# Kernel tuning notes

Measured on AMD Instinct MI355X. Metric: run time of the kernel, lower is better.

Reference implementation:

```python
import jax, jax.numpy as jnp
import numpy as np

B, S, D, H = 2, 2048, 2048, 16
DK = D // H  # 128


def setup_inputs() -> dict:
    key = jax.random.key(0)
    ks = jax.random.split(key, 14)
    scale = 1.0 / np.sqrt(D)
    inp = {
        "query": jax.random.normal(ks[0], (B, S, D), jnp.float32),
        "key": jax.random.normal(ks[1], (B, S, D), jnp.float32),
        "value": jax.random.normal(ks[2], (B, S, D), jnp.float32),
        # Linear params, torch convention: y = x @ W.T + b, W:[out,in]
        "Wq": jax.random.normal(ks[3], (D, D), jnp.float32) * scale,
        "bq": jnp.zeros((D,), jnp.float32),
        "Wk": jax.random.normal(ks[4], (D, D), jnp.float32) * scale,
        "bk": jnp.zeros((D,), jnp.float32),
        "Wv": jax.random.normal(ks[5], (D, D), jnp.float32) * scale,
        "bv": jnp.zeros((D,), jnp.float32),
        "Wo": jax.random.normal(ks[6], (D, D), jnp.float32) * scale,
        "bo": jnp.zeros((D,), jnp.float32),
    }
    return inp


def reference(query, key, value, Wq, bq, Wk, bk, Wv, bv, Wo, bo):
    b, s, d = query.shape
    # QKV projections -> [B, H, S, DK]
    q = (query @ Wq.T + bq).reshape(b, s, H, DK).transpose(0, 2, 1, 3)
    k = (key @ Wk.T + bk).reshape(b, s, H, DK).transpose(0, 2, 1, 3)
    v = (value @ Wv.T + bv).reshape(b, s, H, DK).transpose(0, 2, 1, 3)
    # scaled dot-product scores [B, H, S, S]
    scores = jnp.einsum('bhqd,bhkd->bhqk', q, k) * (1.0 / np.sqrt(DK))
    causal = jnp.tril(jnp.ones((s, s), dtype=bool))  # [S, S], mask==0 above diag
    scores = jnp.where(causal[None, None], scores, jnp.float32(-1e9))
    attn = jax.nn.softmax(scores, axis=-1)  # attn_dropout = identity (eval)
    x = jnp.einsum('bhqk,bhkd->bhqd', attn, v)
    x = x.transpose(0, 2, 1, 3).reshape(b, s, d)
    out = x @ Wo.T + bo  # resid_dropout = identity (eval)
    return (out, attn)
```

## Files before the change

kernel.cpp:

```cpp
#include <hip/hip_runtime.h>


#define BATCH 2
#define S_LEN 2048
#define D_DIM 2048
#define H_NUM 16
#define DKD   128
#define NEL   ((size_t)BATCH * S_LEN * D_DIM)
#define NWL   ((size_t)D_DIM * D_DIM)

typedef __attribute__((ext_vector_type(8))) short  short8;
typedef __attribute__((ext_vector_type(4))) short  short4v;
typedef __attribute__((ext_vector_type(4))) float  floatx4;

__device__ __forceinline__ unsigned short f2bf(float f) {
    unsigned int u = __float_as_uint(f);
    u += 0x7fffu + ((u >> 16) & 1u);
    return (unsigned short)(u >> 16);
}

__device__ __forceinline__ void gload16(const void* g, void* l) {
    __builtin_amdgcn_global_load_lds(
        (const __attribute__((address_space(1))) void*)g,
        (__attribute__((address_space(3))) void*)l, 16, 0, 0);
}

__device__ __forceinline__ void stage_lds_bf16(const unsigned short* __restrict__ src,
                                               int ld, int row0, int k0,
                                               unsigned short* __restrict__ dst,
                                               int tid) {
    #pragma unroll
    for (int j = 0; j < 2; ++j) {
        const int c = tid + j * 256;
        const int r = c >> 2, kc = (c & 3) * 8;
        gload16(src + (size_t)(row0 + r) * ld + k0 + kc, dst + c * 8);
    }
}

__launch_bounds__(256)
__global__ void proj_qkv(const unsigned short* __restrict__ xf,
                         const unsigned short* __restrict__ wb,
                         const float* __restrict__ bq, const float* __restrict__ bk,
                         const float* __restrict__ bv,
                         unsigned short* __restrict__ ob) {
    const int z = blockIdx.z;
    const unsigned short* Ap = xf + (size_t)z * NEL;
    const unsigned short* Bp = wb + (size_t)z * NWL;
    const float* bias = (z == 0) ? bq : (z == 1) ? bk : bv;
    const int m0 = blockIdx.y * 128, n0 = blockIdx.x * 128;

    __shared__ __align__(16) unsigned short As[128][32];
    __shared__ __align__(16) unsigned short Bs[128][32];
    const int tid = threadIdx.x, lane = tid & 63, wave = tid >> 6;
    const int quad = lane >> 4, l16 = lane & 15;
    const int mw = (wave >> 1) * 64, nw = (wave & 1) * 64;

    floatx4 acc[4][4];
    #pragma unroll
    for (int i = 0; i < 4; ++i)
        #pragma unroll
        for (int j = 0; j < 4; ++j) acc[i][j] = (floatx4){0.f, 0.f, 0.f, 0.f};

    for (int k0 = 0; k0 < D_DIM; k0 += 32) {
        if (k0 > 0) __syncthreads();
        stage_lds_bf16(Bp, D_DIM, n0, k0, &Bs[0][0], tid);
        stage_lds_bf16(Ap, D_DIM, m0, k0, &As[0][0], tid);
        __syncthreads();
        short8 af[4], bf[4];
        #pragma unroll
        for (int i = 0; i < 4; ++i) af[i] = *(const short8*)&As[mw + i*16 + l16][quad*8];
        #pragma unroll
        for (int j = 0; j < 4; ++j) bf[j] = *(const short8*)&Bs[nw + j*16 + l16][quad*8];
        #pragma unroll
        for (int i = 0; i < 4; ++i)
            #pragma unroll
            for (int j = 0; j < 4; ++j)
                acc[i][j] = __builtin_amdgcn_mfma_f32_16x16x32_bf16(
                    af[i], bf[j], acc[i][j], 0, 0, 0);
    }

    #pragma unroll
    for (int i = 0; i < 4; ++i)
        #pragma unroll
        for (int j = 0; j < 4; ++j)
            #pragma unroll
            for (int r = 0; r < 4; ++r) {
                const int row = m0 + mw + i*16 + quad*4 + r;
                const int col = n0 + nw + j*16 + l16;
                const float v = acc[i][j][r] + bias[col];
                const int b = row >> 11, s = row & (S_LEN - 1);
                const int h = col >> 7,  dk = col & (DKD - 1);
                if (z < 2) {
                    unsigned short* o = ob + (size_t)z * NEL;
                    o[((size_t)(b * H_NUM + h) * S_LEN + s) * DKD + dk] = f2bf(v);
                } else {
                    unsigned short* o = ob + 2 * NEL;
                    o[((size_t)(b * H_NUM + h) * DKD + dk) * S_LEN + s] = f2bf(v);
                }
            }
}

__launch_bounds__(256)
__global__ void gemm_out(const unsigned short* __restrict__ Ap,
                         const unsigned short* __restrict__ Bp,
                         const float* __restrict__ bias, float* __restrict__ Cg) {
    const int m0 = blockIdx.y * 128, n0 = blockIdx.x * 128;
    __shared__ __align__(16) unsigned short As[128][32];
    __shared__ __align__(16) unsigned short Bs[128][32];
    const int tid = threadIdx.x, lane = tid & 63, wave = tid >> 6;
    const int quad = lane >> 4, l16 = lane & 15;
    const int mw = (wave >> 1) * 64, nw = (wave & 1) * 64;

    floatx4 acc[4][4];
    #pragma unroll
    for (int i = 0; i < 4; ++i)
        #pragma unroll
        for (int j = 0; j < 4; ++j) acc[i][j] = (floatx4){0.f, 0.f, 0.f, 0.f};

    for (int k0 = 0; k0 < D_DIM; k0 += 32) {
        if (k0 > 0) __syncthreads();
        stage_lds_bf16(Bp, D_DIM, n0, k0, &Bs[0][0], tid);
        stage_lds_bf16(Ap, D_DIM, m0, k0, &As[0][0], tid);
        __syncthreads();
        short8 af[4], bf[4];
        #pragma unroll
        for (int i = 0; i < 4; ++i) af[i] = *(const short8*)&As[mw + i*16 + l16][quad*8];
        #pragma unroll
        for (int j = 0; j < 4; ++j) bf[j] = *(const short8*)&Bs[nw + j*16 + l16][quad*8];
        #pragma unroll
        for (int i = 0; i < 4; ++i)
            #pragma unroll
            for (int j = 0; j < 4; ++j)
                acc[i][j] = __builtin_amdgcn_mfma_f32_16x16x32_bf16(
                    af[i], bf[j], acc[i][j], 0, 0, 0);
    }
    #pragma unroll
    for (int i = 0; i < 4; ++i)
        #pragma unroll
        for (int j = 0; j < 4; ++j)
            #pragma unroll
            for (int r = 0; r < 4; ++r) {
                const int row = m0 + mw + i*16 + quad*4 + r;
                const int col = n0 + nw + j*16 + l16;
                Cg[(size_t)row * D_DIM + col] = acc[i][j][r] + bias[col];
            }
}

__launch_bounds__(256)
__global__ void scores_exp(const unsigned short* __restrict__ qb,
                           const unsigned short* __restrict__ kb,
                           float* __restrict__ attn, float* __restrict__ sums,
                           float scale) {
    const int idx = blockIdx.x;
    int mt = (int)((sqrtf(8.f * (float)idx + 1.f) - 1.f) * 0.5f);
    while ((mt + 1) * (mt + 2) / 2 <= idx) ++mt;
    while (mt * (mt + 1) / 2 > idx) --mt;
    const int nt = idx - mt * (mt + 1) / 2;
    const int m0 = mt * 128, n0 = nt * 128;
    const size_t z = blockIdx.z;
    const unsigned short* Ap = qb + z * (size_t)S_LEN * DKD;
    const unsigned short* Bp = kb + z * (size_t)S_LEN * DKD;

    __shared__ __align__(16) unsigned short As[4][128][32];
    __shared__ __align__(16) unsigned short Bs[4][128][32];
    const int tid = threadIdx.x, lane = tid & 63, wave = tid >> 6;
    const int quad = lane >> 4, l16 = lane & 15;
    const int mw = (wave >> 1) * 64, nw = (wave & 1) * 64;

    #pragma unroll
    for (int kk = 0; kk < 4; ++kk) {
        stage_lds_bf16(Ap, DKD, m0, kk * 32, &As[kk][0][0], tid);
        stage_lds_bf16(Bp, DKD, n0, kk * 32, &Bs[kk][0][0], tid);
    }
    __syncthreads();

    floatx4 acc[4][4];
    #pragma unroll
    for (int i = 0; i < 4; ++i)
        #pragma unroll
        for (int j = 0; j < 4; ++j) acc[i][j] = (floatx4){0.f, 0.f, 0.f, 0.f};

    #pragma unroll
    for (int kk = 0; kk < 4; ++kk) {
        short8 af[4], bf[4];
        #pragma unroll
        for (int i = 0; i < 4; ++i) af[i] = *(const short8*)&As[kk][mw + i*16 + l16][quad*8];
        #pragma unroll
        for (int j = 0; j < 4; ++j) bf[j] = *(const short8*)&Bs[kk][nw + j*16 + l16][quad*8];
        #pragma unroll
        for (int i = 0; i < 4; ++i)
            #pragma unroll
            for (int j = 0; j < 4; ++j)
                acc[i][j] = __builtin_amdgcn_mfma_f32_16x16x32_bf16(
                    af[i], bf[j], acc[i][j], 0, 0, 0);
    }

    float* o  = attn + z * (size_t)S_LEN * S_LEN;
    float* sm = sums + z * S_LEN;
    #pragma unroll
    for (int i = 0; i < 4; ++i)
        #pragma unroll
        for (int r = 0; r < 4; ++r) {
            const int row = m0 + mw + i*16 + quad*4 + r;
            float rsum = 0.f;
            #pragma unroll
            for (int j = 0; j < 4; ++j) {
                const int col = n0 + nw + j*16 + l16;
                const float e = (col <= row) ? __expf(acc[i][j][r] * scale) : 0.f;
                o[(size_t)row * S_LEN + col] = e;
                rsum += e;
            }
            rsum += __shfl_xor(rsum, 1, 64);
            rsum += __shfl_xor(rsum, 2, 64);
            rsum += __shfl_xor(rsum, 4, 64);
            rsum += __shfl_xor(rsum, 8, 64);
            if (l16 == 0) atomicAdd(&sm[row], rsum);
        }
}

__launch_bounds__(256)
__global__ void pv_norm(float* __restrict__ attn,
                        const unsigned short* __restrict__ vT,
                        const float* __restrict__ sums,
                        unsigned short* __restrict__ xb) {
    const int mt = (int)gridDim.y - 1 - (int)blockIdx.y;
    const int m0 = mt * 128;
    const size_t z = blockIdx.z;
    float* Sp = attn + z * (size_t)S_LEN * S_LEN;
    const unsigned short* Bp = vT + z * (size_t)DKD * S_LEN;
    const int kEnd = m0 + 128;

    __shared__ __align__(16) unsigned short As[128][32];
    __shared__ __align__(16) unsigned short Bs[128][32];
    __shared__ float inv[128];
    const int tid = threadIdx.x, lane = tid & 63, wave = tid >> 6;
    const int quad = lane >> 4, l16 = lane & 15;
    const int mw = (wave >> 1) * 64, nw = (wave & 1) * 64;

    if (tid < 128) inv[tid] = 1.f / sums[z * S_LEN + m0 + tid];
    __syncthreads();

    floatx4 acc[4][4];
    #pragma unroll
    for (int i = 0; i < 4; ++i)
        #pragma unroll
        for (int j = 0; j < 4; ++j) acc[i][j] = (floatx4){0.f, 0.f, 0.f, 0.f};

    for (int k0 = 0; k0 < kEnd; k0 += 32) {
        if (k0 > 0) __syncthreads();
        stage_lds_bf16(Bp, S_LEN, 0, k0, &Bs[0][0], tid);
        #pragma unroll
        for (int i2 = 0; i2 < 4; ++i2) {
            const int c = tid + i2 * 256;
            const int r = c >> 3, kc = (c & 7) * 4;
            float* p = Sp + (size_t)(m0 + r) * S_LEN + k0 + kc;
            floatx4 v = *(const floatx4*)p;
            const float iv = inv[r];
            floatx4 w;
            w[0] = v[0] * iv; w[1] = v[1] * iv; w[2] = v[2] * iv; w[3] = v[3] * iv;
            *(floatx4*)p = w;
            short4v pk;
            pk[0] = (short)f2bf(w[0]); pk[1] = (short)f2bf(w[1]);
            pk[2] = (short)f2bf(w[2]); pk[3] = (short)f2bf(w[3]);
            *(short4v*)(&As[r][kc]) = pk;
        }
        __syncthreads();
        short8 af[4], bf[4];
        #pragma unroll
        for (int i = 0; i < 4; ++i) af[i] = *(const short8*)&As[mw + i*16 + l16][quad*8];
        #pragma unroll
        for (int j = 0; j < 4; ++j) bf[j] = *(const short8*)&Bs[nw + j*16 + l16][quad*8];
        #pragma unroll
        for (int i = 0; i < 4; ++i)
            #pragma unroll
            for (int j = 0; j < 4; ++j)
                acc[i][j] = __builtin_amdgcn_mfma_f32_16x16x32_bf16(
                    af[i], bf[j], acc[i][j], 0, 0, 0);
    }

    const int b = (int)(z >> 4), h = (int)(z & 15);
    #pragma unroll
    for (int i = 0; i < 4; ++i)
        #pragma unroll
        for (int j = 0; j < 4; ++j)
            #pragma unroll
            for (int r = 0; r < 4; ++r) {
                const int row = m0 + mw + i*16 + quad*4 + r;
                const int col = nw + j*16 + l16;
                xb[((size_t)(b * S_LEN + row)) * D_DIM + h * DKD + col] =
                    f2bf(acc[i][j][r]);
            }

    const int width = S_LEN - kEnd;
    if (width > 0) {
        const floatx4 z4 = {0.f, 0.f, 0.f, 0.f};
        for (int r = 0; r < 128; ++r) {
            float* rp = Sp + (size_t)(m0 + r) * S_LEN + kEnd;
            for (int c = tid * 4; c < width; c += 1024)
                *(floatx4*)(rp + c) = z4;
        }
    }
}

__launch_bounds__(256)
__global__ void cvt3(const float* __restrict__ a, const float* __restrict__ b,
                     const float* __restrict__ c, unsigned short* __restrict__ dst,
                     size_t stride) {
    const float* src = (blockIdx.y == 0) ? a : (blockIdx.y == 1) ? b : c;
    const size_t i = ((size_t)blockIdx.x * 256 + threadIdx.x) * 8;
    const floatx4 x = *(const floatx4*)(src + i);
    const floatx4 y = *(const floatx4*)(src + i + 4);
    short8 o;
    o[0] = (short)f2bf(x[0]); o[1] = (short)f2bf(x[1]);
    o[2] = (short)f2bf(x[2]); o[3] = (short)f2bf(x[3]);
    o[4] = (short)f2bf(y[0]); o[5] = (short)f2bf(y[1]);
    o[6] = (short)f2bf(y[2]); o[7] = (short)f2bf(y[3]);
    *(short8*)(dst + blockIdx.y * stride + i) = o;
}

__launch_bounds__(256)
__global__ void cvt4(const float* __restrict__ a, const float* __restrict__ b,
                     const float* __restrict__ c, const float* __restrict__ d,
                     unsigned short* __restrict__ dst, size_t stride) {
    const float* src = (blockIdx.y == 0) ? a : (blockIdx.y == 1) ? b
                     : (blockIdx.y == 2) ? c : d;
    const size_t i = ((size_t)blockIdx.x * 256 + threadIdx.x) * 8;
    const floatx4 x = *(const floatx4*)(src + i);
    const floatx4 y = *(const floatx4*)(src + i + 4);
    short8 o;
    o[0] = (short)f2bf(x[0]); o[1] = (short)f2bf(x[1]);
    o[2] = (short)f2bf(x[2]); o[3] = (short)f2bf(x[3]);
    o[4] = (short)f2bf(y[0]); o[5] = (short)f2bf(y[1]);
    o[6] = (short)f2bf(y[2]); o[7] = (short)f2bf(y[3]);
    *(short8*)(dst + blockIdx.y * stride + i) = o;
}

__launch_bounds__(256)
__global__ void zero_sums(float* __restrict__ sums) {
    const size_t i = ((size_t)blockIdx.x * 256 + threadIdx.x) * 4;
    *(floatx4*)(sums + i) = (floatx4){0.f, 0.f, 0.f, 0.f};
}

extern "C" void kernel_launch(void* const* d_in, const int* in_sizes, int n_in,
                              void* d_out, int out_size, void* d_ws, size_t ws_size,
                              hipStream_t stream) {
    const float* query = (const float*)d_in[0];
    const float* key_  = (const float*)d_in[1];
    const float* value = (const float*)d_in[2];
    const float* Wq = (const float*)d_in[3];
    const float* bq = (const float*)d_in[4];
    const float* Wk = (const float*)d_in[5];
    const float* bk = (const float*)d_in[6];
    const float* Wv = (const float*)d_in[7];
    const float* bv = (const float*)d_in[8];
    const float* Wo = (const float*)d_in[9];
    const float* bo = (const float*)d_in[10];

    float* out  = (float*)d_out;
    float* attn = out + NEL;

    unsigned short* qb = (unsigned short*)d_ws;
    unsigned short* kb = qb + NEL;
    unsigned short* vT = kb + NEL;
    unsigned short* xb = vT + NEL;
    unsigned short* qf = xb + NEL;
    unsigned short* wq = qf + 3 * NEL;
    unsigned short* wo = wq + 3 * NWL;
    float* sums = (float*)(wo + NWL);

    const dim3 blk(256);
    const float iscale = 0.088388347648318447f;

    cvt3<<<dim3(NEL / 2048, 3), blk, 0, stream>>>(query, key_, value, qf, NEL);
    cvt4<<<dim3(NWL / 2048, 4), blk, 0, stream>>>(Wq, Wk, Wv, Wo, wq, NWL);
    zero_sums<<<dim3((BATCH * H_NUM * S_LEN) / 1024), blk, 0, stream>>>(sums);

    proj_qkv<<<dim3(D_DIM / 128, (BATCH * S_LEN) / 128, 3), blk, 0, stream>>>(
        qf, wq, bq, bk, bv, qb);

    scores_exp<<<dim3(136, 1, BATCH * H_NUM), blk, 0, stream>>>(
        qb, kb, attn, sums, iscale);

    pv_norm<<<dim3(1, S_LEN / 128, BATCH * H_NUM), blk, 0, stream>>>(
        attn, vT, sums, xb);

    gemm_out<<<dim3(D_DIM / 128, (BATCH * S_LEN) / 128), blk, 0, stream>>>(
        xb, wq + 3 * NWL, bo, out);
}
```

Measured before the change: 1.237 ms.

## Fuse scores, softmax and PV into one attention kernel per query block

Replaces the separate scores_exp and pv_norm kernels with a single kernel that works on 32-row query blocks. For each 128-key tile it computes QK^T, exponentiates, writes the unnormalized probabilities, and feeds them as bf16 directly into the PV MFMA. Row sums stay in LDS instead of global atomics, so the zero_sums launch goes away and pv_norm no longer has to re-read attn to build the PV operand. Normalization of the attn output is done in a second pass that re-reads and rewrites the causal part, and zero-filling is folded into the same pass. The costs are smaller tiles with lower MFMA reuse, a row-serial normalization loop, and softmax without max subtraction, as before.

```diff
diff --git a/kernel.cpp b/kernel.cpp
--- a/kernel.cpp
+++ b/kernel.cpp
@@ -6,6 +6,7 @@
 #define D_DIM 2048
 #define H_NUM 16
 #define DKD   128
+#define QBLK  32
 #define NEL   ((size_t)BATCH * S_LEN * D_DIM)
 #define NWL   ((size_t)D_DIM * D_DIM)
 
@@ -147,158 +148,146 @@
 }
 
 __launch_bounds__(256)
-__global__ void scores_exp(const unsigned short* __restrict__ qb,
+__global__ void attn_fused(const unsigned short* __restrict__ qb,
                            const unsigned short* __restrict__ kb,
-                           float* __restrict__ attn, float* __restrict__ sums,
-                           float scale) {
-    const int idx = blockIdx.x;
-    int mt = (int)((sqrtf(8.f * (float)idx + 1.f) - 1.f) * 0.5f);
-    while ((mt + 1) * (mt + 2) / 2 <= idx) ++mt;
-    while (mt * (mt + 1) / 2 > idx) --mt;
-    const int nt = idx - mt * (mt + 1) / 2;
-    const int m0 = mt * 128, n0 = nt * 128;
-    const size_t z = blockIdx.z;
-    const unsigned short* Ap = qb + z * (size_t)S_LEN * DKD;
-    const unsigned short* Bp = kb + z * (size_t)S_LEN * DKD;
-
-    __shared__ __align__(16) unsigned short As[4][128][32];
-    __shared__ __align__(16) unsigned short Bs[4][128][32];
-    const int tid = threadIdx.x, lane = tid & 63, wave = tid >> 6;
+                           const unsigned short* __restrict__ vTg,
+                           float* __restrict__ attn,
+                           unsigned short* __restrict__ xb,
+                           float iscale) {
+    const int bid = blockIdx.x;
+    const int z  = ((bid & 7) << 2) | ((bid >> 3) & 3);
+    const int mt = 63 - (bid >> 5);
+    const int m0 = mt * QBLK;
+    const int nkt = (m0 + QBLK + 127) >> 7;
+    const unsigned short* qz = qb  + (size_t)z * S_LEN * DKD;
+    const unsigned short* kz = kb  + (size_t)z * S_LEN * DKD;
+    const unsigned short* vz = vTg + (size_t)z * DKD * S_LEN;
+    float* az = attn + (size_t)z * S_LEN * S_LEN;
+
+    __shared__ __align__(16) unsigned short Ks[4][128][32];
+    __shared__ __align__(16) unsigned short Vs[4][128][32];
+    __shared__ __align__(16) unsigned short Ps[4][QBLK][32];
+    __shared__ float rsum[QBLK];
+
+    const int tid = threadIdx.x, lane = tid & 63, w = tid >> 6;
     const int quad = lane >> 4, l16 = lane & 15;
-    const int mw = (wave >> 1) * 64, nw = (wave & 1) * 64;
-
-    #pragma unroll
-    for (int kk = 0; kk < 4; ++kk) {
-        stage_lds_bf16(Ap, DKD, m0, kk * 32, &As[kk][0][0], tid);
-        stage_lds_bf16(Bp, DKD, n0, kk * 32, &Bs[kk][0][0], tid);
-    }
-    __syncthreads();
-
-    floatx4 acc[4][4];
-    #pragma unroll
-    for (int i = 0; i < 4; ++i)
-        #pragma unroll
-        for (int j = 0; j < 4; ++j) acc[i][j] = (floatx4){0.f, 0.f, 0.f, 0.f};
-
-    #pragma unroll
-    for (int kk = 0; kk < 4; ++kk) {
-        short8 af[4], bf[4];
-        #pragma unroll
-        for (int i = 0; i < 4; ++i) af[i] = *(const short8*)&As[kk][mw + i*16 + l16][quad*8];
-        #pragma unroll
-        for (int j = 0; j < 4; ++j) bf[j] = *(const short8*)&Bs[kk][nw + j*16 + l16][quad*8];
-        #pragma unroll
-        for (int i = 0; i < 4; ++i)
-            #pragma unroll
-            for (int j = 0; j < 4; ++j)
-                acc[i][j] = __builtin_amdgcn_mfma_f32_16x16x32_bf16(
-                    af[i], bf[j], acc[i][j], 0, 0, 0);
-    }
-
-    float* o  = attn + z * (size_t)S_LEN * S_LEN;
-    float* sm = sums + z * S_LEN;
-    #pragma unroll
-    for (int i = 0; i < 4; ++i)
-        #pragma unroll
-        for (int r = 0; r < 4; ++r) {
-            const int row = m0 + mw + i*16 + quad*4 + r;
-            float rsum = 0.f;
-            #pragma unroll
-            for (int j = 0; j < 4; ++j) {
-                const int col = n0 + nw + j*16 + l16;
-                const float e = (col <= row) ? __expf(acc[i][j][r] * scale) : 0.f;
-                o[(size_t)row * S_LEN + col] = e;
-                rsum += e;
-            }
-            rsum += __shfl_xor(rsum, 1, 64);
-            rsum += __shfl_xor(rsum, 2, 64);
-            rsum += __shfl_xor(rsum, 4, 64);
-            rsum += __shfl_xor(rsum, 8, 64);
-            if (l16 == 0) atomicAdd(&sm[row], rsum);
-        }
-}
-
-__launch_bounds__(256)
-__global__ void pv_norm(float* __restrict__ attn,
-                        const unsigned short* __restrict__ vT,
-                        const float* __restrict__ sums,
-                        unsigned short* __restrict__ xb) {
-    const int mt = (int)gridDim.y - 1 - (int)blockIdx.y;
-    const int m0 = mt * 128;
-    const size_t z = blockIdx.z;
-    float* Sp = attn + z * (size_t)S_LEN * S_LEN;
-    const unsigned short* Bp = vT + z * (size_t)DKD * S_LEN;
-    const int kEnd = m0 + 128;
-
-    __shared__ __align__(16) unsigned short As[128][32];
-    __shared__ __align__(16) unsigned short Bs[128][32];
-    __shared__ float inv[128];
-    const int tid = threadIdx.x, lane = tid & 63, wave = tid >> 6;
-    const int quad = lane >> 4, l16 = lane & 15;
-    const int mw = (wave >> 1) * 64, nw = (wave & 1) * 64;
-
-    if (tid < 128) inv[tid] = 1.f / sums[z * S_LEN + m0 + tid];
-    __syncthreads();
-
-    floatx4 acc[4][4];
-    #pragma unroll
-    for (int i = 0; i < 4; ++i)
-        #pragma unroll
-        for (int j = 0; j < 4; ++j) acc[i][j] = (floatx4){0.f, 0.f, 0.f, 0.f};
-
-    for (int k0 = 0; k0 < kEnd; k0 += 32) {
-        if (k0 > 0) __syncthreads();
-        stage_lds_bf16(Bp, S_LEN, 0, k0, &Bs[0][0], tid);
-        #pragma unroll
-        for (int i2 = 0; i2 < 4; ++i2) {
-            const int c = tid + i2 * 256;
-            const int r = c >> 3, kc = (c & 7) * 4;
-            float* p = Sp + (size_t)(m0 + r) * S_LEN + k0 + kc;
-            floatx4 v = *(const floatx4*)p;
-            const float iv = inv[r];
-            floatx4 w;
-            w[0] = v[0] * iv; w[1] = v[1] * iv; w[2] = v[2] * iv; w[3] = v[3] * iv;
-            *(floatx4*)p = w;
-            short4v pk;
-            pk[0] = (short)f2bf(w[0]); pk[1] = (short)f2bf(w[1]);
-            pk[2] = (short)f2bf(w[2]); pk[3] = (short)f2bf(w[3]);
-            *(short4v*)(&As[r][kc]) = pk;
+
+    if (tid < QBLK) rsum[tid] = 0.f;
+
+    short8 afq[2][4];
+    #pragma unroll
+    for (int i = 0; i < 2; ++i)
+        #pragma unroll
+        for (int kk = 0; kk < 4; ++kk)
+            afq[i][kk] = *(const short8*)(qz + (size_t)(m0 + i*16 + l16) * DKD
+                                             + kk*32 + quad*8);
+
+    floatx4 acc_pv[2][2];
+    #pragma unroll
+    for (int i = 0; i < 2; ++i)
+        #pragma unroll
+        for (int jj = 0; jj < 2; ++jj) acc_pv[i][jj] = (floatx4){0.f,0.f,0.f,0.f};
+    float rp[2][4];
+    #pragma unroll
+    for (int i = 0; i < 2; ++i)
+        #pragma unroll
+        for (int r = 0; r < 4; ++r) rp[i][r] = 0.f;
+
+    for (int kt = 0; kt < nkt; ++kt) {
+        const int k0 = kt * 128;
+        if (kt > 0) __syncthreads();
+        #pragma unroll
+        for (int kk = 0; kk < 4; ++kk) {
+            stage_lds_bf16(kz, DKD,   k0, kk*32,      &Ks[kk][0][0], tid);
+            stage_lds_bf16(vz, S_LEN, 0,  k0 + kk*32, &Vs[kk][0][0], tid);
         }
         __syncthreads();
-        short8 af[4], bf[4];
-        #pragma unroll
-        for (int i = 0; i < 4; ++i) af[i] = *(const short8*)&As[mw + i*16 + l16][quad*8];
-        #pragma unroll
-        for (int j = 0; j < 4; ++j) bf[j] = *(const short8*)&Bs[nw + j*16 + l16][quad*8];
-        #pragma unroll
-        for (int i = 0; i < 4; ++i)
-            #pragma unroll
-            for (int j = 0; j < 4; ++j)
-                acc[i][j] = __builtin_amdgcn_mfma_f32_16x16x32_bf16(
-                    af[i], bf[j], acc[i][j], 0, 0, 0);
-    }
-
-    const int b = (int)(z >> 4), h = (int)(z & 15);
-    #pragma unroll
-    for (int i = 0; i < 4; ++i)
-        #pragma unroll
-        for (int j = 0; j < 4; ++j)
+
+        floatx4 acc_s[2][2];
+        #pragma unroll
+        for (int i = 0; i < 2; ++i)
+            #pragma unroll
+            for (int jj = 0; jj < 2; ++jj) acc_s[i][jj] = (floatx4){0.f,0.f,0.f,0.f};
+        #pragma unroll
+        for (int kk = 0; kk < 4; ++kk)
+            #pragma unroll
+            for (int jj = 0; jj < 2; ++jj) {
+                const short8 bfk = *(const short8*)&Ks[kk][w*32 + jj*16 + l16][quad*8];
+                #pragma unroll
+                for (int i = 0; i < 2; ++i)
+                    acc_s[i][jj] = __builtin_amdgcn_mfma_f32_16x16x32_bf16(
+                        afq[i][kk], bfk, acc_s[i][jj], 0, 0, 0);
+            }
+
+        #pragma unroll
+        for (int i = 0; i < 2; ++i)
+            #pragma unroll
+            for (int jj = 0; jj < 2; ++jj)
+                #pragma unroll
+                for (int r = 0; r < 4; ++r) {
+                    const int row = m0 + i*16 + quad*4 + r;
+                    const int col = k0 + w*32 + jj*16 + l16;
+                    const float e = (col <= row)
+                        ? __expf(acc_s[i][jj][r] * iscale) : 0.f;
+                    az[(size_t)row * S_LEN + col] = e;
+                    rp[i][r] += e;
+                    Ps[w][i*16 + quad*4 + r][jj*16 + l16] = f2bf(e);
+                }
+        __syncthreads();
+
+        #pragma unroll
+        for (int kk = 0; kk < 4; ++kk) {
+            short8 afp[2], bfv[2];
+            #pragma unroll
+            for (int i = 0; i < 2; ++i)
+                afp[i] = *(const short8*)&Ps[kk][i*16 + l16][quad*8];
+            #pragma unroll
+            for (int jj = 0; jj < 2; ++jj)
+                bfv[jj] = *(const short8*)&Vs[kk][w*32 + jj*16 + l16][quad*8];
+            #pragma unroll
+            for (int i = 0; i < 2; ++i)
+                #pragma unroll
+                for (int jj = 0; jj < 2; ++jj)
+                    acc_pv[i][jj] = __builtin_amdgcn_mfma_f32_16x16x32_bf16(
+                        afp[i], bfv[jj], acc_pv[i][jj], 0, 0, 0);
+        }
+    }
+
+    #pragma unroll
+    for (int i = 0; i < 2; ++i)
+        #pragma unroll
+        for (int r = 0; r < 4; ++r) {
+            float v = rp[i][r];
+            v += __shfl_xor(v, 1, 64); v += __shfl_xor(v, 2, 64);
+            v += __shfl_xor(v, 4, 64); v += __shfl_xor(v, 8, 64);
+            if (l16 == 0) atomicAdd(&rsum[i*16 + quad*4 + r], v);
+        }
+    __syncthreads();
+
+    const int b = z >> 4, h = z & 15;
+    #pragma unroll
+    for (int i = 0; i < 2; ++i)
+        #pragma unroll
+        for (int jj = 0; jj < 2; ++jj)
             #pragma unroll
             for (int r = 0; r < 4; ++r) {
-                const int row = m0 + mw + i*16 + quad*4 + r;
-                const int col = nw + j*16 + l16;
-                xb[((size_t)(b * S_LEN + row)) * D_DIM + h * DKD + col] =
-                    f2bf(acc[i][j][r]);
+                const int row = i*16 + quad*4 + r;
+                const float inv = 1.f / rsum[row];
+                xb[((size_t)(b * S_LEN + m0 + row)) * D_DIM
+                   + h*DKD + w*32 + jj*16 + l16] = f2bf(acc_pv[i][jj][r] * inv);
             }
 
-    const int width = S_LEN - kEnd;
-    if (width > 0) {
-        const floatx4 z4 = {0.f, 0.f, 0.f, 0.f};
-        for (int r = 0; r < 128; ++r) {
-            float* rp = Sp + (size_t)(m0 + r) * S_LEN + kEnd;
-            for (int c = tid * 4; c < width; c += 1024)
-                *(floatx4*)(rp + c) = z4;
+    const int ncols4 = nkt * 32;
+    for (int r = 0; r < QBLK; ++r) {
+        const float inv = 1.f / rsum[r];
+        float* rowp = az + (size_t)(m0 + r) * S_LEN;
+        for (int c = tid; c < ncols4; c += 256) {
+            floatx4 v = *(const floatx4*)(rowp + c*4);
+            v[0] *= inv; v[1] *= inv; v[2] *= inv; v[3] *= inv;
+            *(floatx4*)(rowp + c*4) = v;
         }
+        for (int c = ncols4 + tid; c < S_LEN/4; c += 256)
+            *(floatx4*)(rowp + c*4) = (floatx4){0.f,0.f,0.f,0.f};
     }
 }
 
@@ -335,12 +324,6 @@
     *(short8*)(dst + blockIdx.y * stride + i) = o;
 }
 
-__launch_bounds__(256)
-__global__ void zero_sums(float* __restrict__ sums) {
-    const size_t i = ((size_t)blockIdx.x * 256 + threadIdx.x) * 4;
-    *(floatx4*)(sums + i) = (floatx4){0.f, 0.f, 0.f, 0.f};
-}
-
 extern "C" void kernel_launch(void* const* d_in, const int* in_sizes, int n_in,
                               void* d_out, int out_size, void* d_ws, size_t ws_size,
                               hipStream_t stream) {
@@ -366,24 +349,19 @@
     unsigned short* qf = xb + NEL;
     unsigned short* wq = qf + 3 * NEL;
     unsigned short* wo = wq + 3 * NWL;
-    float* sums = (float*)(wo + NWL);
 
     const dim3 blk(256);
     const float iscale = 0.088388347648318447f;
 
     cvt3<<<dim3(NEL / 2048, 3), blk, 0, stream>>>(query, key_, value, qf, NEL);
     cvt4<<<dim3(NWL / 2048, 4), blk, 0, stream>>>(Wq, Wk, Wv, Wo, wq, NWL);
-    zero_sums<<<dim3((BATCH * H_NUM * S_LEN) / 1024), blk, 0, stream>>>(sums);
 
     proj_qkv<<<dim3(D_DIM / 128, (BATCH * S_LEN) / 128, 3), blk, 0, stream>>>(
         qf, wq, bq, bk, bv, qb);
 
-    scores_exp<<<dim3(136, 1, BATCH * H_NUM), blk, 0, stream>>>(
-        qb, kb, attn, sums, iscale);
-
-    pv_norm<<<dim3(1, S_LEN / 128, BATCH * H_NUM), blk, 0, stream>>>(
-        attn, vT, sums, xb);
+    attn_fused<<<dim3(BATCH * H_NUM * (S_LEN / QBLK)), blk, 0, stream>>>(
+        qb, kb, vT, attn, xb, iscale);
 
     gemm_out<<<dim3(D_DIM / 128, (BATCH * S_LEN) / 128), blk, 0, stream>>>(
-        xb, wq + 3 * NWL, bo, out);
-}
+        xb, wo, bo, out);
+}
```

After: 1.099 ms. -11.2%, faster.
